# Performance work log

Hardware: AMD Instinct MI355X
Metric: run time of the kernel (lower is better)

The kernel has to match this reference:

```python
import jax, jax.numpy as jnp
import numpy as np

B, C, T = 4, 512, 2048
STYLE = 128
DEPTH = 4
K = 3               # gated conv kernel size
GN_GROUPS = 4
D_INNER = 2 * C      # mamba expand=2
D_STATE = 16
DT_RANK = 32         # ceil(C/16)
D_CONV = 4
EPS = 1e-5


def conv1d(x, w, groups, pad):
    # x: (B, Cin, T), w: (Cout, Cin//groups, K), pad: (lo, hi)
    return jax.lax.conv_general_dilated(
        x, w, (1,), [pad], dimension_numbers=('NCH', 'OIH', 'NCH'),
        feature_group_count=groups)


def group_norm(x, w, b):
    # x: (B, C, T); GroupNorm(4, C)
    Bn, Cn, Tn = x.shape
    xg = x.reshape(Bn, GN_GROUPS, (Cn // GN_GROUPS) * Tn)
    mu = xg.mean(-1, keepdims=True)
    var = xg.var(-1, keepdims=True)
    xg = (xg - mu) * jax.lax.rsqrt(var + EPS)
    return xg.reshape(Bn, Cn, Tn) * w[None, :, None] + b[None, :, None]


def mamba_block(u, inw, cw, cb, xpw, dpw, dpb, A_log, Dv, opw):
    # u: (B, T, C) -> (B, T, C); standard Mamba selective scan
    xz = u @ inw.T                                   # (B, T, 2*D_INNER)
    xh, z = jnp.split(xz, 2, axis=-1)
    # causal depthwise conv over time
    xc = conv1d(xh.swapaxes(1, 2), cw, D_INNER, (D_CONV - 1, 0)) + cb[None, :, None]
    xc = jax.nn.silu(xc).swapaxes(1, 2)              # (B, T, D_INNER)
    xdbl = xc @ xpw.T                                # (B, T, DT_RANK + 2*D_STATE)
    dt = xdbl[..., :DT_RANK]
    Bm = xdbl[..., DT_RANK:DT_RANK + D_STATE]
    Cm = xdbl[..., DT_RANK + D_STATE:]
    dt = jax.nn.softplus(dt @ dpw.T + dpb)           # (B, T, D_INNER)
    A = -jnp.exp(A_log)                              # (D_INNER, D_STATE)

    def step(h, xs):
        dt_t, B_t, C_t, u_t = xs                     # (B,Di) (B,N) (B,N) (B,Di)
        dA = jnp.exp(dt_t[..., None] * A)            # (B, D_INNER, D_STATE)
        h = h * dA + (dt_t * u_t)[..., None] * B_t[:, None, :]
        y = jnp.einsum('bdn,bn->bd', h, C_t)
        return h, y

    xs = (dt.swapaxes(0, 1), Bm.swapaxes(0, 1), Cm.swapaxes(0, 1), xc.swapaxes(0, 1))
    h0 = jnp.zeros((u.shape[0], D_INNER, D_STATE), u.dtype)
    _, ys = jax.lax.scan(step, h0, xs)               # ys: (T, B, D_INNER)
    y = ys.swapaxes(0, 1) + xc * Dv
    y = y * jax.nn.silu(z)
    return y @ opw.T                                 # (B, T, C)


def setup_inputs() -> dict:
    key = jax.random.key(0)
    ks = jax.random.split(key, 16)
    r = lambda i, shape, s=0.02: jax.random.normal(ks[i], shape, jnp.float32) * s
    A0 = jnp.log(jnp.broadcast_to(
        jnp.arange(1, D_STATE + 1, dtype=jnp.float32), (DEPTH, D_INNER, D_STATE)))
    return {
        'x': jax.random.normal(ks[0], (B, C, T), jnp.float32),
        'style': jax.random.normal(ks[1], (B, STYLE), jnp.float32),
        'conv_w': r(2, (DEPTH, C, 4, K)),            # groups = C//4 -> in/g = 4
        'conv_b': jnp.zeros((DEPTH, C), jnp.float32),
        'gn_w': jnp.ones((DEPTH, C), jnp.float32),
        'gn_b': jnp.zeros((DEPTH, C), jnp.float32),
        'in_proj_w': r(3, (DEPTH, 2 * D_INNER, C)),
        'mconv_w': r(4, (DEPTH, D_INNER, 1, D_CONV), 0.2),
        'mconv_b': jnp.zeros((DEPTH, D_INNER), jnp.float32),
        'x_proj_w': r(5, (DEPTH, DT_RANK + 2 * D_STATE, D_INNER)),
        'dt_proj_w': r(6, (DEPTH, D_INNER, DT_RANK), 0.1),
        'dt_proj_b': r(7, (DEPTH, D_INNER), 0.1),
        'A_log': A0,
        'Dp': jnp.ones((DEPTH, D_INNER), jnp.float32),
        'out_proj_w': r(8, (DEPTH, C, D_INNER)),
        'gate_w': r(9, (2 * C, C, 1)),               # Conv1d(2C,2C,1,groups=2)
        'ln_w': jnp.ones((2 * C,), jnp.float32),
        'ln_b': jnp.zeros((2 * C,), jnp.float32),
        'proj_w': r(10, (C, 2 * C)),
        'm': jnp.zeros((B, T), bool),
    }


def reference(x, style, conv_w, conv_b, gn_w, gn_b, in_proj_w, mconv_w, mconv_b,
              x_proj_w, dt_proj_w, dt_proj_b, A_log, Dp, out_proj_w,
              gate_w, ln_w, ln_b, proj_w, m):
    # stacked gated convs; dropout is identity (eval), weight_norm folded into weight
    h = x
    gsum = jnp.zeros_like(x)
    for i in range(DEPTH):
        h = conv1d(h, conv_w[i], C // 4, ((K - 1) // 2, (K - 1) // 2)) + conv_b[i][None, :, None]
        h = jax.nn.silu(group_norm(h, gn_w[i], gn_b[i]))
        gsum = gsum + h
    gT = gsum.swapaxes(1, 2)                         # (B, T, C)
    mf = jnp.zeros_like(gT)
    for i in range(DEPTH):
        mf = mf + mamba_block(gT, in_proj_w[i], mconv_w[i], mconv_b[i], x_proj_w[i],
                              dt_proj_w[i], dt_proj_b[i], A_log[i], Dp[i], out_proj_w[i])
    combined = jnp.concatenate([gsum, mf.swapaxes(1, 2)], axis=1)   # (B, 2C, T)
    gated = jax.nn.silu(conv1d(combined, gate_w, 2, (0, 0))) * combined
    gt = gated.swapaxes(1, 2)                        # (B, T, 2C)
    mu = gt.mean(-1, keepdims=True)
    var = gt.var(-1, keepdims=True)
    gt = (gt - mu) * jax.lax.rsqrt(var + EPS) * ln_w + ln_b
    out = (gt @ proj_w.T).swapaxes(1, 2)             # (B, C, T)
    return jnp.where(m[:, None, :], 0.0, out)
```

## Files before the change

### kernel.cpp

```cpp
#include <hip/hip_runtime.h>
#include <cstdint>
#include <cstddef>

#define BB 4
#define CC 512
#define TT 2048
#define DINNER 1024
#define DSTATE 16
#define NCH 64
#define NCHSH 6
#define CHL 32
#define MROWS (BB*TT)
#define EPSF 1e-5f

typedef __attribute__((ext_vector_type(8))) short short8;
typedef __attribute__((ext_vector_type(4))) float f32x4;

__device__ __forceinline__ float silu_f(float x) { return x / (1.f + __expf(-x)); }
__device__ __forceinline__ float softplus_f(float x) { return x > 20.f ? x : log1pf(expf(x)); }

__device__ __forceinline__ unsigned short f2bf(float x) {
    union { float f; unsigned u; } v; v.f = x;
    unsigned r = v.u + 0x7FFFu + ((v.u >> 16) & 1u);
    return (unsigned short)(r >> 16);
}
__device__ __forceinline__ float bf2f(unsigned short h) {
    union { unsigned u; float f; } v; v.u = ((unsigned)h) << 16;
    return v.f;
}

template<bool ACC>
__global__ __launch_bounds__(256, 2) void gemm_mfma_k(const float* __restrict__ A,
                                                      const float* __restrict__ W,
                                                      float* __restrict__ C,
                                                      int N, int K)
{
    __shared__ short Ah[128*40], Al[128*40], Bh[128*40], Bl[128*40];
    const int tid = threadIdx.x;
    const int m0 = blockIdx.y << 7, n0 = blockIdx.x << 7;
    const int srow = tid >> 1, skh = (tid & 1) << 4;
    const int wid = tid >> 6, lane = tid & 63;
    const int wr = wid >> 1, wc = wid & 1;
    const int l15 = lane & 15, l4 = lane >> 4;

    f32x4 acc[4][4] = {};

    const float* Ap = A + (size_t)(m0 + srow)*K + skh;
    const float* Wp = W + (size_t)(n0 + srow)*K + skh;
    const int sbase = srow*40 + skh;

    for (int k0 = 0; k0 < K; k0 += 32) {
        {
            f32x4 x0 = *(const f32x4*)(Ap + k0);
            f32x4 x1 = *(const f32x4*)(Ap + k0 + 4);
            f32x4 x2 = *(const f32x4*)(Ap + k0 + 8);
            f32x4 x3 = *(const f32x4*)(Ap + k0 + 12);
            float xs[16] = {x0[0],x0[1],x0[2],x0[3], x1[0],x1[1],x1[2],x1[3],
                            x2[0],x2[1],x2[2],x2[3], x3[0],x3[1],x3[2],x3[3]};
            unsigned hp[8], lp[8];
            #pragma unroll
            for (int p = 0; p < 8; ++p) {
                unsigned short h0 = f2bf(xs[2*p]),   h1 = f2bf(xs[2*p+1]);
                unsigned short g0 = f2bf(xs[2*p]   - bf2f(h0));
                unsigned short g1 = f2bf(xs[2*p+1] - bf2f(h1));
                hp[p] = (unsigned)h0 | ((unsigned)h1 << 16);
                lp[p] = (unsigned)g0 | ((unsigned)g1 << 16);
            }
            *(uint4*)&Ah[sbase]     = make_uint4(hp[0],hp[1],hp[2],hp[3]);
            *(uint4*)&Ah[sbase + 8] = make_uint4(hp[4],hp[5],hp[6],hp[7]);
            *(uint4*)&Al[sbase]     = make_uint4(lp[0],lp[1],lp[2],lp[3]);
            *(uint4*)&Al[sbase + 8] = make_uint4(lp[4],lp[5],lp[6],lp[7]);
        }
        {
            f32x4 x0 = *(const f32x4*)(Wp + k0);
            f32x4 x1 = *(const f32x4*)(Wp + k0 + 4);
            f32x4 x2 = *(const f32x4*)(Wp + k0 + 8);
            f32x4 x3 = *(const f32x4*)(Wp + k0 + 12);
            float xs[16] = {x0[0],x0[1],x0[2],x0[3], x1[0],x1[1],x1[2],x1[3],
                            x2[0],x2[1],x2[2],x2[3], x3[0],x3[1],x3[2],x3[3]};
            unsigned hp[8], lp[8];
            #pragma unroll
            for (int p = 0; p < 8; ++p) {
                unsigned short h0 = f2bf(xs[2*p]),   h1 = f2bf(xs[2*p+1]);
                unsigned short g0 = f2bf(xs[2*p]   - bf2f(h0));
                unsigned short g1 = f2bf(xs[2*p+1] - bf2f(h1));
                hp[p] = (unsigned)h0 | ((unsigned)h1 << 16);
                lp[p] = (unsigned)g0 | ((unsigned)g1 << 16);
            }
            *(uint4*)&Bh[sbase]     = make_uint4(hp[0],hp[1],hp[2],hp[3]);
            *(uint4*)&Bh[sbase + 8] = make_uint4(hp[4],hp[5],hp[6],hp[7]);
            *(uint4*)&Bl[sbase]     = make_uint4(lp[0],lp[1],lp[2],lp[3]);
            *(uint4*)&Bl[sbase + 8] = make_uint4(lp[4],lp[5],lp[6],lp[7]);
        }
        __syncthreads();

        const int abase = (wr*64 + l15)*40 + l4*8;
        const int bbase = (wc*64 + l15)*40 + l4*8;
        short8 ah[4], al[4], bh[4], bl[4];
        #pragma unroll
        for (int i = 0; i < 4; ++i) {
            ah[i] = *(const short8*)&Ah[abase + i*640];
            al[i] = *(const short8*)&Al[abase + i*640];
            bh[i] = *(const short8*)&Bh[bbase + i*640];
            bl[i] = *(const short8*)&Bl[bbase + i*640];
        }
        #pragma unroll
        for (int i = 0; i < 4; ++i)
            #pragma unroll
            for (int j = 0; j < 4; ++j) {
                acc[i][j] = __builtin_amdgcn_mfma_f32_16x16x32_bf16(ah[i], bh[j], acc[i][j], 0, 0, 0);
                acc[i][j] = __builtin_amdgcn_mfma_f32_16x16x32_bf16(ah[i], bl[j], acc[i][j], 0, 0, 0);
                acc[i][j] = __builtin_amdgcn_mfma_f32_16x16x32_bf16(al[i], bh[j], acc[i][j], 0, 0, 0);
            }
        __syncthreads();
    }

    #pragma unroll
    for (int i = 0; i < 4; ++i) {
        #pragma unroll
        for (int j = 0; j < 4; ++j) {
            const int col  = n0 + wc*64 + j*16 + l15;
            const int rowb = m0 + wr*64 + i*16 + l4*4;
            float* cp = C + (size_t)rowb*N + col;
            #pragma unroll
            for (int r = 0; r < 4; ++r) {
                float v = acc[i][j][r];
                if constexpr (ACC) v += cp[(size_t)r*N];
                cp[(size_t)r*N] = v;
            }
        }
    }
}

template<int EPI, bool ACC>
__global__ __launch_bounds__(256) void gemm_k(const float* __restrict__ A, int lda,
                                              const float* __restrict__ W,
                                              float* __restrict__ C,
                                              int N, int K,
                                              const float* __restrict__ bias)
{
    __shared__ float As[16][68];
    __shared__ float Bs[16][68];
    const int tid = threadIdx.x;
    const int tx = tid & 15, ty = tid >> 4;
    const int m0 = blockIdx.y << 6, n0 = blockIdx.x << 6;
    const int lk4 = tid & 3, lrow = tid >> 2;
    float acc[4][4] = {};
    for (int k0 = 0; k0 < K; k0 += 16) {
        float4 av = *(const float4*)(A + (size_t)(m0 + lrow)*lda + k0 + lk4*4);
        float4 bv = *(const float4*)(W + (size_t)(n0 + lrow)*K  + k0 + lk4*4);
        As[lk4*4+0][lrow] = av.x; As[lk4*4+1][lrow] = av.y;
        As[lk4*4+2][lrow] = av.z; As[lk4*4+3][lrow] = av.w;
        Bs[lk4*4+0][lrow] = bv.x; Bs[lk4*4+1][lrow] = bv.y;
        Bs[lk4*4+2][lrow] = bv.z; Bs[lk4*4+3][lrow] = bv.w;
        __syncthreads();
        #pragma unroll
        for (int k = 0; k < 16; ++k) {
            const float4 a = *(const float4*)(&As[k][ty << 2]);
            const float4 b = *(const float4*)(&Bs[k][tx << 2]);
            float ar[4] = {a.x, a.y, a.z, a.w};
            float br[4] = {b.x, b.y, b.z, b.w};
            #pragma unroll
            for (int i = 0; i < 4; ++i)
                #pragma unroll
                for (int j = 0; j < 4; ++j)
                    acc[i][j] = fmaf(ar[i], br[j], acc[i][j]);
        }
        __syncthreads();
    }
    #pragma unroll
    for (int i = 0; i < 4; ++i) {
        int m = m0 + (ty << 2) + i;
        float* cp = C + (size_t)m*N + n0 + (tx << 2);
        float4 v = make_float4(acc[i][0], acc[i][1], acc[i][2], acc[i][3]);
        if constexpr (EPI == 1) {
            const float4 b4 = *(const float4*)(bias + n0 + (tx << 2));
            v.x = softplus_f(v.x + b4.x); v.y = softplus_f(v.y + b4.y);
            v.z = softplus_f(v.z + b4.z); v.w = softplus_f(v.w + b4.w);
        }
        if constexpr (ACC) {
            float4 o = *(const float4*)cp;
            v.x += o.x; v.y += o.y; v.z += o.z; v.w += o.w;
        }
        *(float4*)cp = v;
    }
}

__global__ __launch_bounds__(256) void front_conv_k(const float* __restrict__ in,
                                                    const float* __restrict__ w,
                                                    const float* __restrict__ cb,
                                                    float* __restrict__ out)
{
    int idx = blockIdx.x*256 + threadIdx.x;
    int t = idx & (TT-1);
    int bc = idx >> 11;
    int c = bc & (CC-1);
    const float* wr = w + c*12;
    const float* base = in + ((size_t)(bc & ~3) << 11) + t;
    float s = cb[c];
    #pragma unroll
    for (int i = 0; i < 4; ++i) {
        const float* ip = base + ((size_t)i << 11);
        float a = wr[i*3+1]*ip[0];
        if (t > 0)     a += wr[i*3+0]*ip[-1];
        if (t < TT-1)  a += wr[i*3+2]*ip[1];
        s += a;
    }
    out[idx] = s;
}

__global__ __launch_bounds__(256) void gn_stats_k(const float* __restrict__ x, float* __restrict__ red)
{
    int pair  = blockIdx.x >> 4;
    int slice = blockIdx.x & 15;
    const float* base = x + ((size_t)pair << 18);
    float s = 0.f, s2 = 0.f;
    int i0 = slice*16384 + threadIdx.x;
    int iend = slice*16384 + 16384;
    for (int i = i0; i < iend; i += 256) { float v = base[i]; s += v; s2 += v*v; }
    for (int off = 32; off > 0; off >>= 1) { s += __shfl_down(s, off, 64); s2 += __shfl_down(s2, off, 64); }
    __shared__ float sb[4][2];
    int wid = threadIdx.x >> 6, lane = threadIdx.x & 63;
    if (lane == 0) { sb[wid][0] = s; sb[wid][1] = s2; }
    __syncthreads();
    if (threadIdx.x == 0) {
        s  = sb[0][0]+sb[1][0]+sb[2][0]+sb[3][0];
        s2 = sb[0][1]+sb[1][1]+sb[2][1]+sb[3][1];
        atomicAdd(&red[pair*2+0], s);
        atomicAdd(&red[pair*2+1], s2);
    }
}

template<bool FIRST>
__global__ __launch_bounds__(256) void gn_apply_k(float* __restrict__ h, float* __restrict__ gsum,
    const float* __restrict__ red, const float* __restrict__ gw, const float* __restrict__ gb)
{
    int idx = blockIdx.x*256 + threadIdx.x;
    int c = (idx >> 11) & (CC-1);
    int pair = idx >> 18;
    const float inv = 1.f/262144.f;
    float mu = red[pair*2]*inv;
    float var = red[pair*2+1]*inv - mu*mu;
    float rs = rsqrtf(var + EPSF);
    float v = (h[idx]-mu)*rs*gw[c]+gb[c];
    float sv = v / (1.f + expf(-v));
    h[idx] = sv;
    gsum[idx] = FIRST ? sv : (gsum[idx] + sv);
}

template<bool MASK>
__global__ void transpose_k(const float* __restrict__ src, float* __restrict__ dst,
                            int R, int Cl, const unsigned char* __restrict__ msk)
{
    __shared__ float tile[32][33];
    int b = blockIdx.z;
    int r0 = blockIdx.y << 5, c0 = blockIdx.x << 5;
    const float* s = src + (size_t)b*R*Cl;
    float* d = dst + (size_t)b*R*Cl;
    int tx = threadIdx.x, ty = threadIdx.y;
    #pragma unroll
    for (int j = 0; j < 32; j += 8) tile[ty+j][tx] = s[(size_t)(r0+ty+j)*Cl + c0+tx];
    __syncthreads();
    bool mz = false;
    if (MASK) mz = msk[(size_t)b*R + r0 + tx] != 0;
    #pragma unroll
    for (int j = 0; j < 32; j += 8) {
        float v = tile[tx][ty+j];
        if (MASK && mz) v = 0.f;
        d[(size_t)(c0+ty+j)*R + r0+tx] = v;
    }
}

__global__ __launch_bounds__(256) void mamba_conv_k(const float* __restrict__ xz,
    const float* __restrict__ w, const float* __restrict__ cb, float* __restrict__ xc)
{
    int idx = blockIdx.x*256 + threadIdx.x;
    int d = idx & (DINNER-1);
    int bt = idx >> 10;
    int t = bt & (TT-1);
    const float* wd = w + d*4;
    const float* src = xz + ((size_t)bt << 11) + d;
    float s = cb[d];
    #pragma unroll
    for (int k = 0; k < 4; ++k) {
        int dtt = k - 3;
        if (t + dtt >= 0) s += wd[k] * src[(ptrdiff_t)dtt << 11];
    }
    xc[idx] = silu_f(s);
}

__global__ __launch_bounds__(256) void scan_p1_k(const float* __restrict__ dt, const float* __restrict__ xc,
    const float* __restrict__ xdbl, const float* __restrict__ Alog,
    float* __restrict__ ch_h, float* __restrict__ ch_sd)
{
    int idx = blockIdx.x*256 + threadIdx.x;
    int d = idx & 1023;
    int bc = idx >> 10;
    int ch = bc & (NCH-1);
    int b = bc >> NCHSH;
    float Ad[16];
    #pragma unroll
    for (int n = 0; n < 16; ++n) Ad[n] = -__expf(Alog[d*16+n]);
    float h[16];
    #pragma unroll
    for (int n = 0; n < 16; ++n) h[n] = 0.f;
    float sd = 0.f;
    size_t rbase = (size_t)(b*TT + ch*CHL);
    const float* dtp = dt + (rbase << 10) + d;
    const float* xcp = xc + (rbase << 10) + d;
    const float* xdp = xdbl + rbase*64 + 32;
    for (int tt = 0; tt < CHL; ++tt) {
        float dtv = dtp[(size_t)tt << 10];
        float u   = xcp[(size_t)tt << 10];
        sd += dtv;
        float du = dtv*u;
        const float* Bv = xdp + tt*64;
        #pragma unroll
        for (int n = 0; n < 16; ++n) h[n] = h[n]*__expf(dtv*Ad[n]) + du*Bv[n];
    }
    float* hp = ch_h + ((size_t)idx << 4);
    #pragma unroll
    for (int n = 0; n < 16; ++n) hp[n] = h[n];
    ch_sd[idx] = sd;
}

__global__ __launch_bounds__(256) void scan_p2_k(const float* __restrict__ Alog, const float* __restrict__ ch_h,
    const float* __restrict__ ch_sd, float* __restrict__ hinit)
{
    int idx = blockIdx.x*256 + threadIdx.x;
    int dn = idx & 16383;
    int b = idx >> 14;
    int d = dn >> 4;
    float A = -__expf(Alog[dn]);
    float h = 0.f;
    for (int ch = 0; ch < NCH; ++ch) {
        size_t o = ((size_t)((b*NCH + ch)) << 14) + dn;
        hinit[o] = h;
        h = h*__expf(A*ch_sd[((b*NCH+ch) << 10) + d]) + ch_h[o];
    }
}

__global__ __launch_bounds__(256) void scan_p3_k(const float* __restrict__ dt, const float* __restrict__ xc,
    const float* __restrict__ xdbl, const float* __restrict__ Alog, const float* __restrict__ hinit,
    const float* __restrict__ xz, const float* __restrict__ Dp, float* __restrict__ y)
{
    int idx = blockIdx.x*256 + threadIdx.x;
    int d = idx & 1023;
    int bc = idx >> 10;
    int ch = bc & (NCH-1);
    int b = bc >> NCHSH;
    float Ad[16];
    #pragma unroll
    for (int n = 0; n < 16; ++n) Ad[n] = -__expf(Alog[d*16+n]);
    float h[16];
    const float* hp = hinit + ((size_t)idx << 4);
    #pragma unroll
    for (int n = 0; n < 16; ++n) h[n] = hp[n];
    float Dv = Dp[d];
    size_t rbase = (size_t)(b*TT + ch*CHL);
    const float* dtp = dt + (rbase << 10) + d;
    const float* xcp = xc + (rbase << 10) + d;
    const float* xdp = xdbl + rbase*64;
    const float* zp  = xz + (rbase << 11) + 1024 + d;
    float* yp = y + (rbase << 10) + d;
    for (int tt = 0; tt < CHL; ++tt) {
        float dtv = dtp[(size_t)tt << 10];
        float u   = xcp[(size_t)tt << 10];
        float du = dtv*u;
        const float* Bv = xdp + tt*64 + 32;
        const float* Cv = xdp + tt*64 + 48;
        float acc = 0.f;
        #pragma unroll
        for (int n = 0; n < 16; ++n) {
            h[n] = h[n]*__expf(dtv*Ad[n]) + du*Bv[n];
            acc += h[n]*Cv[n];
        }
        float z = zp[(size_t)tt << 11];
        yp[(size_t)tt << 10] = (acc + u*Dv) * silu_f(z);
    }
}

__global__ __launch_bounds__(256) void gate_ln_k(const float* __restrict__ G1, const float* __restrict__ G2,
    const float* __restrict__ u, const float* __restrict__ mf,
    const float* __restrict__ lnw, const float* __restrict__ lnb, float* __restrict__ gt)
{
    int m = blockIdx.x;
    int tid = threadIdx.x;
    __shared__ float buf[1024];
    __shared__ float sb[4][2];
    __shared__ float stats[2];
    float s = 0.f, s2 = 0.f;
    #pragma unroll
    for (int c = tid; c < 1024; c += 256) {
        float g, comb;
        if (c < 512) { g = G1[(size_t)m*512 + c];       comb = u [(size_t)m*512 + c]; }
        else         { g = G2[(size_t)m*512 + c - 512]; comb = mf[(size_t)m*512 + c - 512]; }
        float v = (g / (1.f + expf(-g))) * comb;
        buf[c] = v;
        s += v; s2 += v*v;
    }
    for (int off = 32; off > 0; off >>= 1) { s += __shfl_down(s, off, 64); s2 += __shfl_down(s2, off, 64); }
    int wid = tid >> 6, lane = tid & 63;
    if (lane == 0) { sb[wid][0] = s; sb[wid][1] = s2; }
    __syncthreads();
    if (tid == 0) {
        float S  = sb[0][0]+sb[1][0]+sb[2][0]+sb[3][0];
        float S2 = sb[0][1]+sb[1][1]+sb[2][1]+sb[3][1];
        float mu = S*(1.f/1024.f);
        float var = S2*(1.f/1024.f) - mu*mu;
        stats[0] = mu; stats[1] = rsqrtf(var + EPSF);
    }
    __syncthreads();
    float mu = stats[0], rs = stats[1];
    #pragma unroll
    for (int c = tid; c < 1024; c += 256)
        gt[(size_t)m*1024 + c] = (buf[c]-mu)*rs*lnw[c] + lnb[c];
}

extern "C" void kernel_launch(void* const* d_in, const int* in_sizes, int n_in,
                              void* d_out, int out_size, void* d_ws, size_t ws_size,
                              hipStream_t stream)
{
    (void)in_sizes; (void)n_in; (void)out_size; (void)ws_size;
    const float* x        = (const float*)d_in[0];
    const float* conv_w   = (const float*)d_in[2];
    const float* conv_b   = (const float*)d_in[3];
    const float* gn_w     = (const float*)d_in[4];
    const float* gn_b     = (const float*)d_in[5];
    const float* in_projw = (const float*)d_in[6];
    const float* mconv_w  = (const float*)d_in[7];
    const float* mconv_b  = (const float*)d_in[8];
    const float* x_projw  = (const float*)d_in[9];
    const float* dt_projw = (const float*)d_in[10];
    const float* dt_projb = (const float*)d_in[11];
    const float* A_log    = (const float*)d_in[12];
    const float* Dp       = (const float*)d_in[13];
    const float* out_projw= (const float*)d_in[14];
    const float* gate_w   = (const float*)d_in[15];
    const float* ln_w     = (const float*)d_in[16];
    const float* ln_b     = (const float*)d_in[17];
    const float* proj_w   = (const float*)d_in[18];
    const unsigned char* msk = (const unsigned char*)d_in[19];
    float* out = (float*)d_out;
    float* ws  = (float*)d_ws;

    const size_t NEL = (size_t)BB*CC*TT;
    const size_t NCHW = (size_t)BB*NCH*DINNER;
    float* gsum = ws;
    float* hA   = gsum + NEL;
    float* hB   = hA + NEL;
    float* mf   = hB + NEL;
    float* xz   = mf + NEL;
    float* xc   = xz + (size_t)MROWS*2048;
    float* xdbl = xc + (size_t)MROWS*1024;
    float* dtb  = xdbl + (size_t)MROWS*64;
    float* yb   = dtb + (size_t)MROWS*1024;
    float* red  = yb + (size_t)MROWS*1024;
    float* ch_sd= red + 64;
    float* ch_h = hA;
    float* hinit= gsum;
    float* G1  = xz;
    float* G2  = xz + NEL;
    float* gt  = xc;
    float* gt2 = yb;
    float* u   = hB;

    const float* cur_in = x;
    float* pp[2] = {hB, hA};
    for (int i = 0; i < 4; ++i) {
        float* co = pp[i & 1];
        front_conv_k<<<16384, 256, 0, stream>>>(cur_in, conv_w + (size_t)i*CC*12, conv_b + i*CC, co);
        hipMemsetAsync(red, 0, 32*sizeof(float), stream);
        gn_stats_k<<<256, 256, 0, stream>>>(co, red);
        if (i == 0) gn_apply_k<true ><<<16384, 256, 0, stream>>>(co, gsum, red, gn_w + i*CC, gn_b + i*CC);
        else        gn_apply_k<false><<<16384, 256, 0, stream>>>(co, gsum, red, gn_w + i*CC, gn_b + i*CC);
        cur_in = co;
    }

    transpose_k<false><<<dim3(64,16,4), dim3(32,8), 0, stream>>>(gsum, u, CC, TT, nullptr);

    for (int i = 0; i < 4; ++i) {
        gemm_mfma_k<false><<<dim3(16,64), 256, 0, stream>>>(u, in_projw + (size_t)i*2048*512, xz, 2048, 512);
        mamba_conv_k<<<32768, 256, 0, stream>>>(xz, mconv_w + (size_t)i*DINNER*4, mconv_b + i*DINNER, xc);
        gemm_k<0,false><<<dim3(1,128), 256, 0, stream>>>(xc, 1024, x_projw + (size_t)i*64*1024, xdbl, 64, 1024, nullptr);
        gemm_k<1,false><<<dim3(16,128), 256, 0, stream>>>(xdbl, 64, dt_projw + (size_t)i*1024*32, dtb, 1024, 32, dt_projb + i*1024);
        scan_p1_k<<<NCHW/256, 256, 0, stream>>>(dtb, xc, xdbl, A_log + (size_t)i*16384, ch_h, ch_sd);
        scan_p2_k<<<256, 256, 0, stream>>>(A_log + (size_t)i*16384, ch_h, ch_sd, hinit);
        scan_p3_k<<<NCHW/256, 256, 0, stream>>>(dtb, xc, xdbl, A_log + (size_t)i*16384, hinit, xz, Dp + i*DINNER, yb);
        if (i == 0) gemm_mfma_k<false><<<dim3(4,64), 256, 0, stream>>>(yb, out_projw + (size_t)i*512*1024, mf, 512, 1024);
        else        gemm_mfma_k<true ><<<dim3(4,64), 256, 0, stream>>>(yb, out_projw + (size_t)i*512*1024, mf, 512, 1024);
    }

    gemm_mfma_k<false><<<dim3(4,64), 256, 0, stream>>>(u,  gate_w,           G1, 512, 512);
    gemm_mfma_k<false><<<dim3(4,64), 256, 0, stream>>>(mf, gate_w + 512*512, G2, 512, 512);
    gate_ln_k<<<8192, 256, 0, stream>>>(G1, G2, u, mf, ln_w, ln_b, gt);
    gemm_mfma_k<false><<<dim3(4,64), 256, 0, stream>>>(gt, proj_w, gt2, 512, 1024);
    transpose_k<true><<<dim3(16,64,4), dim3(32,8), 0, stream>>>(gt2, out, TT, CC, msk);
}
```

Before: 2.109 ms.

## Pre-split GEMM operands into bf16 hi/lo pairs once, outside the GEMM inner loops

Adds a kernel that splits fp32 tensors into bf16 high and low halves. It applies it to the weights, the transposed activations and the merged mamba output. The scan and gate/LayerNorm kernels now write split bf16 outputs directly. A new GEMM loads the pre-split operands with 128-bit copies and runs three bf16 MFMAs per tile. The out-projection and gate GEMMs use a narrower 64-column tile so more blocks run. This removes the fp32-to-bf16 conversion from the GEMM loops, at the cost of extra workspace, extra split passes and the weights being re-split on every call. The path runs only when the workspace is large enough.

```diff
diff --git a/kernel.cpp b/kernel.cpp
--- a/kernel.cpp
+++ b/kernel.cpp
@@ -27,6 +27,101 @@
 __device__ __forceinline__ float bf2f(unsigned short h) {
     union { unsigned u; float f; } v; v.u = ((unsigned)h) << 16;
     return v.f;
+}
+
+__global__ __launch_bounds__(256) void split_bf16_k(const float* __restrict__ in,
+    unsigned short* __restrict__ hi, unsigned short* __restrict__ lo, int n8)
+{
+    for (int i = blockIdx.x*256 + threadIdx.x; i < n8; i += gridDim.x*256) {
+        const f32x4* p = (const f32x4*)in + 2*(size_t)i;
+        f32x4 a = p[0], b = p[1];
+        float xs[8] = {a[0],a[1],a[2],a[3], b[0],b[1],b[2],b[3]};
+        unsigned h[8], l[8];
+        #pragma unroll
+        for (int q = 0; q < 8; ++q) {
+            unsigned short hh = f2bf(xs[q]);
+            h[q] = hh;
+            l[q] = f2bf(xs[q] - bf2f(hh));
+        }
+        ((uint4*)hi)[i] = make_uint4(h[0]|(h[1]<<16), h[2]|(h[3]<<16), h[4]|(h[5]<<16), h[6]|(h[7]<<16));
+        ((uint4*)lo)[i] = make_uint4(l[0]|(l[1]<<16), l[2]|(l[3]<<16), l[4]|(l[5]<<16), l[6]|(l[7]<<16));
+    }
+}
+
+template<int BNT, bool ACC>
+__global__ __launch_bounds__(256, 2) void gemm_bf16s_k(const unsigned short* __restrict__ Ahg,
+    const unsigned short* __restrict__ Alg,
+    const unsigned short* __restrict__ Whg, const unsigned short* __restrict__ Wlg,
+    float* __restrict__ C, int N, int K)
+{
+    constexpr int NJ = BNT/32;
+    constexpr int LDT = 40;
+    __shared__ short Ah[128*LDT], Al[128*LDT], Bh[BNT*LDT], Bl[BNT*LDT];
+    const int tid = threadIdx.x;
+    const int m0 = blockIdx.y << 7, n0 = blockIdx.x * BNT;
+    const int srow = tid >> 2, scol = (tid & 3) << 3;
+    const int wid = tid >> 6, lane = tid & 63;
+    const int wr = wid >> 1, wc = wid & 1;
+    const int l15 = lane & 15, l4 = lane >> 4;
+
+    f32x4 acc[4][NJ] = {};
+
+    for (int k0 = 0; k0 < K; k0 += 32) {
+        size_t ga = (size_t)(m0 + srow)*K + k0 + scol;
+        *(uint4*)&Ah[srow*LDT + scol] = *(const uint4*)(Ahg + ga);
+        *(uint4*)&Al[srow*LDT + scol] = *(const uint4*)(Alg + ga);
+        size_t ga2 = ga + (size_t)64*K;
+        *(uint4*)&Ah[(srow+64)*LDT + scol] = *(const uint4*)(Ahg + ga2);
+        *(uint4*)&Al[(srow+64)*LDT + scol] = *(const uint4*)(Alg + ga2);
+        size_t gb = (size_t)(n0 + srow)*K + k0 + scol;
+        *(uint4*)&Bh[srow*LDT + scol] = *(const uint4*)(Whg + gb);
+        *(uint4*)&Bl[srow*LDT + scol] = *(const uint4*)(Wlg + gb);
+        if constexpr (BNT == 128) {
+            size_t gb2 = gb + (size_t)64*K;
+            *(uint4*)&Bh[(srow+64)*LDT + scol] = *(const uint4*)(Whg + gb2);
+            *(uint4*)&Bl[(srow+64)*LDT + scol] = *(const uint4*)(Wlg + gb2);
+        }
+        __syncthreads();
+
+        short8 ah[4], al[4], bh[NJ], bl[NJ];
+        const int ab = (wr*64 + l15)*LDT + l4*8;
+        #pragma unroll
+        for (int i = 0; i < 4; ++i) {
+            ah[i] = *(const short8*)&Ah[ab + i*16*LDT];
+            al[i] = *(const short8*)&Al[ab + i*16*LDT];
+        }
+        const int bb = (wc*(BNT/2) + l15)*LDT + l4*8;
+        #pragma unroll
+        for (int j = 0; j < NJ; ++j) {
+            bh[j] = *(const short8*)&Bh[bb + j*16*LDT];
+            bl[j] = *(const short8*)&Bl[bb + j*16*LDT];
+        }
+        #pragma unroll
+        for (int i = 0; i < 4; ++i)
+            #pragma unroll
+            for (int j = 0; j < NJ; ++j) {
+                acc[i][j] = __builtin_amdgcn_mfma_f32_16x16x32_bf16(ah[i], bh[j], acc[i][j], 0, 0, 0);
+                acc[i][j] = __builtin_amdgcn_mfma_f32_16x16x32_bf16(ah[i], bl[j], acc[i][j], 0, 0, 0);
+                acc[i][j] = __builtin_amdgcn_mfma_f32_16x16x32_bf16(al[i], bh[j], acc[i][j], 0, 0, 0);
+            }
+        __syncthreads();
+    }
+
+    #pragma unroll
+    for (int i = 0; i < 4; ++i) {
+        #pragma unroll
+        for (int j = 0; j < NJ; ++j) {
+            const int col  = n0 + wc*(BNT/2) + j*16 + l15;
+            const int rowb = m0 + wr*64 + i*16 + l4*4;
+            float* cp = C + (size_t)rowb*N + col;
+            #pragma unroll
+            for (int r = 0; r < 4; ++r) {
+                float v = acc[i][j][r];
+                if constexpr (ACC) v += cp[(size_t)r*N];
+                cp[(size_t)r*N] = v;
+            }
+        }
+    }
 }
 
 template<bool ACC>
@@ -340,9 +435,11 @@
     }
 }
 
+template<int BF>
 __global__ __launch_bounds__(256) void scan_p3_k(const float* __restrict__ dt, const float* __restrict__ xc,
     const float* __restrict__ xdbl, const float* __restrict__ Alog, const float* __restrict__ hinit,
-    const float* __restrict__ xz, const float* __restrict__ Dp, float* __restrict__ y)
+    const float* __restrict__ xz, const float* __restrict__ Dp, float* __restrict__ y,
+    unsigned short* __restrict__ yh, unsigned short* __restrict__ yl)
 {
     int idx = blockIdx.x*256 + threadIdx.x;
     int d = idx & 1023;
@@ -362,7 +459,6 @@
     const float* xcp = xc + (rbase << 10) + d;
     const float* xdp = xdbl + rbase*64;
     const float* zp  = xz + (rbase << 11) + 1024 + d;
-    float* yp = y + (rbase << 10) + d;
     for (int tt = 0; tt < CHL; ++tt) {
         float dtv = dtp[(size_t)tt << 10];
         float u   = xcp[(size_t)tt << 10];
@@ -376,13 +472,23 @@
             acc += h[n]*Cv[n];
         }
         float z = zp[(size_t)tt << 11];
-        yp[(size_t)tt << 10] = (acc + u*Dv) * silu_f(z);
-    }
-}
-
+        float yv = (acc + u*Dv) * silu_f(z);
+        size_t o = ((rbase + tt) << 10) + d;
+        if constexpr (BF == 0) {
+            y[o] = yv;
+        } else {
+            unsigned short hh = f2bf(yv);
+            yh[o] = hh;
+            yl[o] = f2bf(yv - bf2f(hh));
+        }
+    }
+}
+
+template<int BF>
 __global__ __launch_bounds__(256) void gate_ln_k(const float* __restrict__ G1, const float* __restrict__ G2,
     const float* __restrict__ u, const float* __restrict__ mf,
-    const float* __restrict__ lnw, const float* __restrict__ lnb, float* __restrict__ gt)
+    const float* __restrict__ lnw, const float* __restrict__ lnb,
+    float* __restrict__ gt, unsigned short* __restrict__ gth, unsigned short* __restrict__ gtl)
 {
     int m = blockIdx.x;
     int tid = threadIdx.x;
@@ -413,15 +519,24 @@
     __syncthreads();
     float mu = stats[0], rs = stats[1];
     #pragma unroll
-    for (int c = tid; c < 1024; c += 256)
-        gt[(size_t)m*1024 + c] = (buf[c]-mu)*rs*lnw[c] + lnb[c];
+    for (int c = tid; c < 1024; c += 256) {
+        float v = (buf[c]-mu)*rs*lnw[c] + lnb[c];
+        size_t o = (size_t)m*1024 + c;
+        if constexpr (BF == 0) {
+            gt[o] = v;
+        } else {
+            unsigned short hh = f2bf(v);
+            gth[o] = hh;
+            gtl[o] = f2bf(v - bf2f(hh));
+        }
+    }
 }
 
 extern "C" void kernel_launch(void* const* d_in, const int* in_sizes, int n_in,
                               void* d_out, int out_size, void* d_ws, size_t ws_size,
                               hipStream_t stream)
 {
-    (void)in_sizes; (void)n_in; (void)out_size; (void)ws_size;
+    (void)in_sizes; (void)n_in; (void)out_size;
     const float* x        = (const float*)d_in[0];
     const float* conv_w   = (const float*)d_in[2];
     const float* conv_b   = (const float*)d_in[3];
@@ -461,9 +576,32 @@
     float* hinit= gsum;
     float* G1  = xz;
     float* G2  = xz + NEL;
+    float* u   = hB;
+
+    const size_t IPW_E = (size_t)4*2048*512;
+    const size_t OPW_E = (size_t)4*512*1024;
+    const size_t GW_E  = (size_t)1024*512;
+    const size_t PW_E  = (size_t)512*1024;
+    unsigned short* ush = (unsigned short*)(ch_sd + NCHW);
+    unsigned short* uhp  = ush;                 unsigned short* ulp  = uhp  + NEL;
+    unsigned short* ipwh = ulp + NEL;           unsigned short* ipwl = ipwh + IPW_E;
+    unsigned short* opwh = ipwl + IPW_E;        unsigned short* opwl = opwh + OPW_E;
+    unsigned short* gwh  = opwl + OPW_E;        unsigned short* gwl  = gwh  + GW_E;
+    unsigned short* pwh  = gwl + GW_E;          unsigned short* pwl  = pwh  + PW_E;
+    size_t req = (size_t)((unsigned short*)(pwl + PW_E) - (unsigned short*)ws) * 2;
+    const bool pathA = (ws_size >= req);
+    unsigned short* ybh = (unsigned short*)yb;  unsigned short* ybl = ybh + (size_t)MROWS*1024;
+    unsigned short* mfh = (unsigned short*)hA;  unsigned short* mfl = mfh + NEL;
+    unsigned short* gth = (unsigned short*)yb;  unsigned short* gtl = gth + (size_t)MROWS*1024;
+    float* gt2 = pathA ? xc : yb;
     float* gt  = xc;
-    float* gt2 = yb;
-    float* u   = hB;
+
+    if (pathA) {
+        split_bf16_k<<<2048, 256, 0, stream>>>(in_projw,  ipwh, ipwl, (int)(IPW_E/8));
+        split_bf16_k<<<1024, 256, 0, stream>>>(out_projw, opwh, opwl, (int)(OPW_E/8));
+        split_bf16_k<<< 256, 256, 0, stream>>>(gate_w,    gwh,  gwl,  (int)(GW_E/8));
+        split_bf16_k<<< 256, 256, 0, stream>>>(proj_w,    pwh,  pwl,  (int)(PW_E/8));
+    }
 
     const float* cur_in = x;
     float* pp[2] = {hB, hA};
@@ -478,22 +616,45 @@
     }
 
     transpose_k<false><<<dim3(64,16,4), dim3(32,8), 0, stream>>>(gsum, u, CC, TT, nullptr);
+    if (pathA) split_bf16_k<<<2048, 256, 0, stream>>>(u, uhp, ulp, (int)(NEL/8));
 
     for (int i = 0; i < 4; ++i) {
-        gemm_mfma_k<false><<<dim3(16,64), 256, 0, stream>>>(u, in_projw + (size_t)i*2048*512, xz, 2048, 512);
+        if (pathA)
+            gemm_bf16s_k<128,false><<<dim3(16,64), 256, 0, stream>>>(uhp, ulp,
+                ipwh + (size_t)i*2048*512, ipwl + (size_t)i*2048*512, xz, 2048, 512);
+        else
+            gemm_mfma_k<false><<<dim3(16,64), 256, 0, stream>>>(u, in_projw + (size_t)i*2048*512, xz, 2048, 512);
         mamba_conv_k<<<32768, 256, 0, stream>>>(xz, mconv_w + (size_t)i*DINNER*4, mconv_b + i*DINNER, xc);
         gemm_k<0,false><<<dim3(1,128), 256, 0, stream>>>(xc, 1024, x_projw + (size_t)i*64*1024, xdbl, 64, 1024, nullptr);
         gemm_k<1,false><<<dim3(16,128), 256, 0, stream>>>(xdbl, 64, dt_projw + (size_t)i*1024*32, dtb, 1024, 32, dt_projb + i*1024);
         scan_p1_k<<<NCHW/256, 256, 0, stream>>>(dtb, xc, xdbl, A_log + (size_t)i*16384, ch_h, ch_sd);
         scan_p2_k<<<256, 256, 0, stream>>>(A_log + (size_t)i*16384, ch_h, ch_sd, hinit);
-        scan_p3_k<<<NCHW/256, 256, 0, stream>>>(dtb, xc, xdbl, A_log + (size_t)i*16384, hinit, xz, Dp + i*DINNER, yb);
-        if (i == 0) gemm_mfma_k<false><<<dim3(4,64), 256, 0, stream>>>(yb, out_projw + (size_t)i*512*1024, mf, 512, 1024);
-        else        gemm_mfma_k<true ><<<dim3(4,64), 256, 0, stream>>>(yb, out_projw + (size_t)i*512*1024, mf, 512, 1024);
-    }
-
-    gemm_mfma_k<false><<<dim3(4,64), 256, 0, stream>>>(u,  gate_w,           G1, 512, 512);
-    gemm_mfma_k<false><<<dim3(4,64), 256, 0, stream>>>(mf, gate_w + 512*512, G2, 512, 512);
-    gate_ln_k<<<8192, 256, 0, stream>>>(G1, G2, u, mf, ln_w, ln_b, gt);
-    gemm_mfma_k<false><<<dim3(4,64), 256, 0, stream>>>(gt, proj_w, gt2, 512, 1024);
+        if (pathA) {
+            scan_p3_k<1><<<NCHW/256, 256, 0, stream>>>(dtb, xc, xdbl, A_log + (size_t)i*16384, hinit, xz,
+                                                       Dp + i*DINNER, nullptr, ybh, ybl);
+            if (i == 0) gemm_bf16s_k<64,false><<<dim3(8,64), 256, 0, stream>>>(ybh, ybl,
+                            opwh + (size_t)i*512*1024, opwl + (size_t)i*512*1024, mf, 512, 1024);
+            else        gemm_bf16s_k<64,true ><<<dim3(8,64), 256, 0, stream>>>(ybh, ybl,
+                            opwh + (size_t)i*512*1024, opwl + (size_t)i*512*1024, mf, 512, 1024);
+        } else {
+            scan_p3_k<0><<<NCHW/256, 256, 0, stream>>>(dtb, xc, xdbl, A_log + (size_t)i*16384, hinit, xz,
+                                                       Dp + i*DINNER, yb, nullptr, nullptr);
+            if (i == 0) gemm_mfma_k<false><<<dim3(4,64), 256, 0, stream>>>(yb, out_projw + (size_t)i*512*1024, mf, 512, 1024);
+            else        gemm_mfma_k<true ><<<dim3(4,64), 256, 0, stream>>>(yb, out_projw + (size_t)i*512*1024, mf, 512, 1024);
+        }
+    }
+
+    if (pathA) {
+        split_bf16_k<<<2048, 256, 0, stream>>>(mf, mfh, mfl, (int)(NEL/8));
+        gemm_bf16s_k<64,false><<<dim3(8,64), 256, 0, stream>>>(uhp, ulp, gwh, gwl, G1, 512, 512);
+        gemm_bf16s_k<64,false><<<dim3(8,64), 256, 0, stream>>>(mfh, mfl, gwh + (size_t)512*512, gwl + (size_t)512*512, G2, 512, 512);
+        gate_ln_k<1><<<8192, 256, 0, stream>>>(G1, G2, u, mf, ln_w, ln_b, nullptr, gth, gtl);
+        gemm_bf16s_k<64,false><<<dim3(8,64), 256, 0, stream>>>(gth, gtl, pwh, pwl, gt2, 512, 1024);
+    } else {
+        gemm_mfma_k<false><<<dim3(4,64), 256, 0, stream>>>(u,  gate_w,           G1, 512, 512);
+        gemm_mfma_k<false><<<dim3(4,64), 256, 0, stream>>>(mf, gate_w + 512*512, G2, 512, 512);
+        gate_ln_k<0><<<8192, 256, 0, stream>>>(G1, G2, u, mf, ln_w, ln_b, gt, nullptr, nullptr);
+        gemm_mfma_k<false><<<dim3(4,64), 256, 0, stream>>>(gt, proj_w, gt2, 512, 1024);
+    }
     transpose_k<true><<<dim3(16,64,4), dim3(32,8), 0, stream>>>(gt2, out, TT, CC, msk);
 }
```

After: 2.094 ms. Within noise of the previous version (-0.7%).
